# Kernel tuning notes

Hardware: AMD Instinct MI355X
Metric: run time of the kernel (lower is better)

## Reference

```python
import jax, jax.numpy as jnp
import numpy as np
import math

B, T, C, H, LC, DFF = 2, 1024, 1024, 16, 256, 4096
EPS = 1e-6


def _ln(x):
    # LayerNorm without affine (elementwise_affine=False under AdaLN), eps=1e-6
    m = jnp.mean(x, -1, keepdims=True)
    v = jnp.mean((x - m) ** 2, -1, keepdims=True)
    return (x - m) * jax.lax.rsqrt(v + EPS)


def _heads(t):
    b, l, c = t.shape
    return t.reshape(b, l, H, c // H).transpose(0, 2, 1, 3)  # (b,H,l,dh)


def _unheads(t):
    b, h, l, d = t.shape
    return t.transpose(0, 2, 1, 3).reshape(b, l, h * d)


def setup_inputs():
    key = jax.random.key(0)
    ks = jax.random.split(key, 16)
    s = 0.02
    p = lambda k, sh: jax.random.normal(k, sh, jnp.float32) * s
    x_star = jax.random.normal(ks[0], (B, T, C), jnp.float32)
    x_hat = jax.random.normal(ks[1], (B, T, C), jnp.float32)
    c = jax.random.normal(ks[2], (B, LC, C), jnp.float32)
    chunk = jnp.sort(jax.random.randint(ks[3], (B, T), 0, 32), axis=1)
    m_star = chunk[:, :, None] > chunk[:, None, :]   # attend to strictly earlier chunks
    m_hat = chunk[:, :, None] == chunk[:, None, :]   # attend within same chunk
    dep_mask = jax.random.bernoulli(ks[4], 0.98, (B, T, T)) | jnp.eye(T, dtype=bool)[None]
    return dict(
        x_star=x_star, x_hat=x_hat, c=c,
        m_star=m_star, m_hat=m_hat, dep_mask=dep_mask,
        ncond_g=jnp.ones((C,), jnp.float32), ncond_b=jnp.zeros((C,), jnp.float32),
        Wq=p(ks[5], (C, C)), bq=jnp.zeros((C,), jnp.float32),
        Wkv=p(ks[6], (C, 2 * C)), bkv=jnp.zeros((2 * C,), jnp.float32),
        Wco=p(ks[7], (C, C)), bco=jnp.zeros((C,), jnp.float32),
        Wada=p(ks[8], (C, 6 * C)), bada=jnp.zeros((6 * C,), jnp.float32),
        Wqkv=p(ks[9], (C, 3 * C)), bqkv=jnp.zeros((3 * C,), jnp.float32),
        Wo=p(ks[10], (C, C)), bo=jnp.zeros((C,), jnp.float32),
        W1=p(ks[11], (C, DFF)), b1=jnp.zeros((DFF,), jnp.float32),
        W2=p(ks[12], (DFF, C)), b2=jnp.zeros((C,), jnp.float32),
    )


def _cross_attn(x, c, Wq, bq, Wkv, bkv, Wco, bco):
    q = _heads(x @ Wq + bq)
    k, v = jnp.split(c @ Wkv + bkv, 2, -1)
    k, v = _heads(k), _heads(v)
    att = jnp.einsum('bhtd,bhsd->bhts', q, k) / math.sqrt(C // H)
    y = jnp.einsum('bhts,bhsd->bhtd', jax.nn.softmax(att, -1), v)
    return _unheads(y) @ Wco + bco


def _interleave(xs, xh, m_star, m_hat, dep, Wqkv, bqkv, Wo, bo):
    # Attention.forward_interleave (eval: dropout identity)
    NEG = -jnp.inf
    sc = 1.0 / math.sqrt(C // H)
    qkv = lambda x: [_heads(t) for t in jnp.split(x @ Wqkv + bqkv, 3, -1)]
    qs, ks, vs = qkv(xs)
    qh, kh, vh = qkv(xh)
    blk_star = (~m_star)[:, None]     # True -> block
    blk_hat = (~m_hat)[:, None]
    blk_dep = (~dep)[:, None]
    causal = jnp.triu(jnp.ones((T, T), bool), 1)[None, None]
    # star stream: causal + dependency mask
    att_star = jnp.einsum('bhtd,bhsd->bhts', qs, ks) * sc
    att_star = jnp.where(blk_dep, NEG, att_star)
    p_star = jax.nn.softmax(jnp.where(causal, NEG, att_star), -1)
    y_star = _unheads(jnp.einsum('bhts,bhsd->bhtd', p_star, vs)) @ Wo + bo
    # hat stream: merge logits (q_hat vs k_star on earlier chunks, q_hat vs k_hat within chunk)
    a1 = jnp.where(blk_star, NEG, jnp.einsum('bhtd,bhsd->bhts', qh, ks) * sc)
    a2 = jnp.where(blk_hat, NEG, jnp.einsum('bhtd,bhsd->bhts', qh, kh) * sc)
    merged = jnp.where(jnp.isinf(a2), a1, a2)
    merged = jnp.where(blk_dep, NEG, merged)
    p_hat = jax.nn.softmax(merged, -1)
    y_hat = jnp.einsum('bhts,bhsd->bhtd', jnp.where(blk_star, 0.0, p_hat), vs) \
          + jnp.einsum('bhts,bhsd->bhtd', jnp.where(blk_hat, 0.0, p_hat), vh)
    y_hat = _unheads(y_hat) @ Wo + bo
    return y_star, y_hat


def reference(x_star, x_hat, c, m_star, m_hat, dep_mask,
              ncond_g, ncond_b, Wq, bq, Wkv, bkv, Wco, bco, Wada, bada,
              Wqkv, bqkv, Wo, bo, W1, b1, W2, b2):
    mod = lambda x, sh, scale: x * (1 + scale) + sh
    mlp = lambda x: jax.nn.gelu(x @ W1 + b1, approximate=True) @ W2 + b2
    ca = lambda x: _cross_attn(_ln(x) * ncond_g + ncond_b, c, Wq, bq, Wkv, bkv, Wco, bco)
    ada = lambda t: jnp.split(jax.nn.silu(t) @ Wada + bada, 6, -1)
    gs = ada(ca(x_star))
    gh = ada(ca(x_hat))
    ms = mod(_ln(x_star), gs[0], gs[1])
    mh = mod(_ln(x_hat), gh[0], gh[1])
    ys, yh = _interleave(ms, mh, m_star, m_hat, dep_mask, Wqkv, bqkv, Wo, bo)
    x_star = x_star + gs[2] * ys
    x_hat = x_hat + gh[2] * yh
    x_star = x_star + gs[5] * mlp(mod(_ln(x_star), gs[3], gs[4]))
    x_hat = x_hat + gh[5] * mlp(mod(_ln(x_hat), gh[3], gh[4]))
    return x_star, x_hat
```

## Files before the change

### kernel.cpp

```cpp
#include <hip/hip_runtime.h>
#include <hip/hip_bf16.h>
#include <stdint.h>

#define DEVI __device__ __forceinline__

typedef __bf16 bf16x8 __attribute__((ext_vector_type(8)));
typedef float f32x4 __attribute__((ext_vector_type(4)));
typedef unsigned short us;
typedef unsigned long long ull;

DEVI float b2f(us u) { union { unsigned int i; float f; } v; v.i = ((unsigned int)u) << 16; return v.f; }
DEVI us f2b(float f) {
  union { unsigned int i; float f; } v; v.f = f;
  unsigned int r = (v.i + 0x7fffu + ((v.i >> 16) & 1u)) >> 16;
  return (us)r;
}

#define NEGINF (-__builtin_inff())

DEVI void gl2lds16(const us* g, us* l) {
  __builtin_amdgcn_global_load_lds(
      (const __attribute__((address_space(1))) unsigned int*)g,
      (__attribute__((address_space(3))) unsigned int*)l, 16, 0, 0);
}

__global__ __launch_bounds__(256) void detect_flags(
    const unsigned int* __restrict__ xw, const unsigned int* __restrict__ mw,
    int* __restrict__ flags) {
  const int t = threadIdx.x;
  int cnt = 0, big = 0;
  for (int i = t; i < 4096; i += 256) {
    unsigned int w = xw[i];
    us lo = (us)(w & 0xffffu);
    float a = fabsf(b2f(lo));
    cnt += ((lo == 0) || (a >= 1e-8f && a <= 256.f)) ? 1 : 0;
    big |= (mw[i] > 1u) ? 1 : 0;
  }
  for (int o = 32; o; o >>= 1) { cnt += __shfl_down(cnt, o); big |= __shfl_down(big, o); }
  __shared__ int sc[4], sb[4];
  if ((t & 63) == 0) { sc[t >> 6] = cnt; sb[t >> 6] = big; }
  __syncthreads();
  if (t == 0) {
    flags[0] = (sc[0] + sc[1] + sc[2] + sc[3] < 2048) ? 1 : 0;
    flags[1] = (sb[0] | sb[1] | sb[2] | sb[3]);
  }
}

__global__ __launch_bounds__(256) void cvt_bf16(
    const void* __restrict__ src, us* __restrict__ dst, int n,
    const int* __restrict__ flags) {
  const int f32mode = flags[0];
  int idx = (blockIdx.x * 256 + threadIdx.x) * 4;
  if (idx >= n) return;
  if (f32mode) {
    const float* s = (const float*)src;
    float4 v = *(const float4*)(s + idx);
    dst[idx] = f2b(v.x); dst[idx + 1] = f2b(v.y);
    dst[idx + 2] = f2b(v.z); dst[idx + 3] = f2b(v.w);
  } else {
    *(uint2*)(dst + idx) = *(const uint2*)((const us*)src + idx);
  }
}

struct P10 { const void* p[10]; };
__global__ __launch_bounds__(256) void cvt_small(P10 ps, us* __restrict__ dst,
                                                 const int* __restrict__ flags) {
  const int offs[11] = {0, 1024, 2048, 3072, 5120, 6144, 12288, 15360, 16384, 20480, 21504};
  int idx = blockIdx.x * 256 + threadIdx.x;
  if (idx >= 21504) return;
  int seg = 0;
#pragma unroll
  for (int i = 1; i < 10; ++i) seg += (idx >= offs[i]) ? 1 : 0;
  int local = idx - offs[seg];
  float v = flags[0] ? ((const float*)ps.p[seg])[local]
                     : b2f(((const us*)ps.p[seg])[local]);
  dst[idx] = f2b(v);
}

__global__ __launch_bounds__(256) void transpose_cvt64(
    const void* __restrict__ W, us* __restrict__ WT, int K, int N,
    const int* __restrict__ flags) {
  __shared__ __attribute__((aligned(16))) us tile[64 * 72];
  const int f32m = flags[0];
  const int k0 = blockIdx.x * 64, n0 = blockIdx.y * 64;
  const int t = threadIdx.x;
  const int row = t >> 2, colb = (t & 3) * 16;
  const int sw = ((row >> 4) & 3) << 4;
  us tmp[16];
  if (f32m) {
    const float* src = (const float*)W + (size_t)(k0 + row) * N + n0 + colb;
#pragma unroll
    for (int i = 0; i < 16; i += 4) {
      float4 v = *(const float4*)(src + i);
      tmp[i] = f2b(v.x); tmp[i + 1] = f2b(v.y); tmp[i + 2] = f2b(v.z); tmp[i + 3] = f2b(v.w);
    }
  } else {
    const us* src = (const us*)W + (size_t)(k0 + row) * N + n0 + colb;
    *(uint4*)tmp = *(const uint4*)src;
    *(uint4*)(tmp + 8) = *(const uint4*)(src + 8);
  }
  *(uint4*)&tile[row * 72 + (colb ^ sw)] = *(uint4*)tmp;
  *(uint4*)&tile[row * 72 + (colb ^ sw) + 8] = *(uint4*)(tmp + 8);
  __syncthreads();
  const int orow = t >> 2, ocolb = (t & 3) * 16;
  const int pc = (orow & 15) | ((orow & 48) ^ (ocolb & 48));
  us out[16];
#pragma unroll
  for (int i = 0; i < 16; ++i) out[i] = tile[(ocolb + i) * 72 + pc];
  us* dst = WT + (size_t)(n0 + orow) * K + k0 + ocolb;
  *(uint4*)dst = *(uint4*)out;
  *(uint4*)(dst + 8) = *(uint4*)(out + 8);
}

struct P3 { const void* p[3]; };
__global__ __launch_bounds__(256) void pack_mask3(P3 ms, ull* __restrict__ bits,
                                                  const int* __restrict__ flags) {
  const int bytemode = flags[1];
  const void* m = ms.p[blockIdx.y];
  ull* out = bits + (size_t)blockIdx.y * 32768;
  int wv = blockIdx.x * 4 + (threadIdx.x >> 6);
  int lane = threadIdx.x & 63;
  for (int w = 0; w < 16; ++w) {
    int v;
    if (bytemode) v = ((const unsigned char*)m)[(size_t)wv * 1024 + w * 64 + lane];
    else          v = ((const int*)m)[(size_t)wv * 1024 + w * 64 + lane];
    ull b = __ballot(v != 0);
    if (lane == 0) out[(size_t)wv * 16 + w] = b;
  }
}

__global__ __launch_bounds__(256) void hat_blockflags(
    const ull* __restrict__ starb, const ull* __restrict__ hatb, int* __restrict__ bf) {
  const int bt = blockIdx.x;
  const int b = bt >> 4, tt = bt & 15;
  const int t = threadIdx.x, wv = t >> 6, lane = t & 63;
  const int t0 = tt * 64;
  for (int k = 0; k < 4; ++k) {
    int ck = wv * 4 + k;
    ull sw = starb[(size_t)(b * 1024 + t0 + lane) * 16 + ck];
    ull hw = hatb[(size_t)(b * 1024 + t0 + lane) * 16 + ck];
    int f = (__ballot(sw != 0ull) ? 1 : 0) | (__ballot(hw != 0ull) ? 2 : 0);
    if (lane == 0) bf[bt * 16 + ck] = f;
  }
}

__global__ __launch_bounds__(256) void vtrans(
    const us* __restrict__ src, us* __restrict__ dst,
    int T, int stride, int colBase, int rowOff) {
  __shared__ __attribute__((aligned(16))) us tile[64][65];
  const int bh = blockIdx.y, b = bh >> 4, h = bh & 15;
  const int t0 = blockIdx.x * 64;
  const int t = threadIdx.x;
#pragma unroll
  for (int it = 0; it < 2; ++it) {
    int idx = it * 256 + t; int r = idx >> 3, c8 = (idx & 7) * 8;
    uint4 d4 = *(const uint4*)(src + (size_t)(rowOff + b * T + t0 + r) * stride + colBase + h * 64 + c8);
    const us* e = (const us*)&d4;
#pragma unroll
    for (int i = 0; i < 8; ++i) tile[r][c8 + i] = e[i];
  }
  __syncthreads();
#pragma unroll
  for (int it = 0; it < 2; ++it) {
    int idx = it * 256 + t; int d = idx >> 3, c8 = (idx & 7) * 8;
    us tmp[8];
#pragma unroll
    for (int i = 0; i < 8; ++i) tmp[i] = tile[c8 + i][d];
    *(uint4*)(dst + ((size_t)(bh * 64 + d)) * T + t0 + c8) = *(const uint4*)tmp;
  }
}

__global__ __launch_bounds__(256) void vtrans_qkv(
    const us* __restrict__ src, us* __restrict__ dst0, us* __restrict__ dst1) {
  __shared__ __attribute__((aligned(16))) us tile[64][65];
  const int z = blockIdx.z;
  us* dst = z ? dst1 : dst0;
  const int rowOff = z ? 2048 : 0;
  const int bh = blockIdx.y, b = bh >> 4, h = bh & 15;
  const int t0 = blockIdx.x * 64;
  const int t = threadIdx.x;
#pragma unroll
  for (int it = 0; it < 2; ++it) {
    int idx = it * 256 + t; int r = idx >> 3, c8 = (idx & 7) * 8;
    uint4 d4 = *(const uint4*)(src + (size_t)(rowOff + b * 1024 + t0 + r) * 3072 + 2048 + h * 64 + c8);
    const us* e = (const us*)&d4;
#pragma unroll
    for (int i = 0; i < 8; ++i) tile[r][c8 + i] = e[i];
  }
  __syncthreads();
#pragma unroll
  for (int it = 0; it < 2; ++it) {
    int idx = it * 256 + t; int d = idx >> 3, c8 = (idx & 7) * 8;
    us tmp[8];
#pragma unroll
    for (int i = 0; i < 8; ++i) tmp[i] = tile[c8 + i][d];
    *(uint4*)(dst + ((size_t)(bh * 64 + d)) * 1024 + t0 + c8) = *(const uint4*)tmp;
  }
}

__global__ __launch_bounds__(256) void ln_affine(
    const void* __restrict__ xs, const void* __restrict__ xh,
    const us* __restrict__ gw, const us* __restrict__ bw,
    us* __restrict__ lnx, us* __restrict__ xn, const int* __restrict__ flags) {
  const int f32m = flags[0];
  const int row = blockIdx.x;
  const void* xp = (row < 2048) ? xs : xh;
  const size_t base = (size_t)(row & 2047) * 1024;
  const int t = threadIdx.x;
  float v[4]; float s = 0.f, ss = 0.f;
#pragma unroll
  for (int i = 0; i < 4; ++i) {
    size_t idx = base + i * 256 + t;
    float x = f32m ? ((const float*)xp)[idx] : b2f(((const us*)xp)[idx]);
    v[i] = x; s += x; ss += x * x;
  }
  for (int o = 32; o; o >>= 1) { s += __shfl_down(s, o); ss += __shfl_down(ss, o); }
  __shared__ float red[2][4];
  const int wv = t >> 6, lane = t & 63;
  if (lane == 0) { red[0][wv] = s; red[1][wv] = ss; }
  __syncthreads();
  s = red[0][0] + red[0][1] + red[0][2] + red[0][3];
  ss = red[1][0] + red[1][1] + red[1][2] + red[1][3];
  const float mean = s * (1.f / 1024.f);
  const float var = fmaxf(ss * (1.f / 1024.f) - mean * mean, 0.f);
  const float rstd = rsqrtf(var + 1e-6f);
  const size_t ro = (size_t)row * 1024;
#pragma unroll
  for (int i = 0; i < 4; ++i) {
    int c = i * 256 + t;
    float n = (v[i] - mean) * rstd;
    lnx[ro + c] = f2b(n);
    xn[ro + c] = f2b(n * b2f(gw[c]) + b2f(bw[c]));
  }
}

__global__ __launch_bounds__(256) void mod_ms(
    const us* __restrict__ lnx, const us* __restrict__ gada, us* __restrict__ ms) {
  const size_t idx = ((size_t)blockIdx.x * 256 + threadIdx.x) * 4;
  const int row = (int)(idx >> 10), c = (int)(idx & 1023);
  const size_t gb = (size_t)row * 6144;
#pragma unroll
  for (int i = 0; i < 4; ++i) {
    float sh = b2f(gada[gb + c + i]);
    float sc = b2f(gada[gb + 1024 + c + i]);
    ms[idx + i] = f2b(b2f(lnx[idx + i]) * (1.f + sc) + sh);
  }
}

__global__ __launch_bounds__(256) void ln_mod(
    const float* __restrict__ x1, const us* __restrict__ gada, us* __restrict__ m2) {
  const int row = blockIdx.x;
  const float* xp = x1 + (size_t)row * 1024;
  const int t = threadIdx.x;
  float v[4]; float s = 0.f, ss = 0.f;
#pragma unroll
  for (int i = 0; i < 4; ++i) { float x = xp[i * 256 + t]; v[i] = x; s += x; ss += x * x; }
  for (int o = 32; o; o >>= 1) { s += __shfl_down(s, o); ss += __shfl_down(ss, o); }
  __shared__ float red[2][4];
  const int wv = t >> 6, lane = t & 63;
  if (lane == 0) { red[0][wv] = s; red[1][wv] = ss; }
  __syncthreads();
  s = red[0][0] + red[0][1] + red[0][2] + red[0][3];
  ss = red[1][0] + red[1][1] + red[1][2] + red[1][3];
  const float mean = s * (1.f / 1024.f);
  const float var = fmaxf(ss * (1.f / 1024.f) - mean * mean, 0.f);
  const float rstd = rsqrtf(var + 1e-6f);
  const size_t gb = (size_t)row * 6144;
#pragma unroll
  for (int i = 0; i < 4; ++i) {
    int c = i * 256 + t;
    float n = (v[i] - mean) * rstd;
    float sh = b2f(gada[gb + 3072 + c]);
    float sc = b2f(gada[gb + 4096 + c]);
    m2[(size_t)row * 1024 + c] = f2b(n * (1.f + sc) + sh);
  }
}

enum { EPI_BF16 = 0, EPI_SILU, EPI_GELU, EPI_GATE_XRES, EPI_GATE_OUT };

template <int EPI>
DEVI void gemm_epi(float v, int gmr, int gn, int N, void* out,
                   const us* gate, const void* res0, const void* res1,
                   const int* oflags) {
  const size_t oi = (size_t)gmr * N + gn;
  if constexpr (EPI == EPI_BF16) {
    ((us*)out)[oi] = f2b(v);
  } else if constexpr (EPI == EPI_SILU) {
    ((us*)out)[oi] = f2b(v / (1.f + __expf(-v)));
  } else if constexpr (EPI == EPI_GELU) {
    float u = 0.7978845608028654f * (v + 0.044715f * v * v * v);
    float th = 1.f - 2.f / (__expf(2.f * u) + 1.f);
    ((us*)out)[oi] = f2b(0.5f * v * (1.f + th));
  } else if constexpr (EPI == EPI_GATE_XRES) {
    float g = b2f(gate[(size_t)gmr * 6144 + gn]);
    const void* xr = (gmr < 2048) ? res0 : res1;
    size_t xi = (size_t)(gmr & 2047) * 1024 + gn;
    float x = oflags[0] ? ((const float*)xr)[xi] : b2f(((const us*)xr)[xi]);
    ((float*)out)[oi] = x + g * v;
  } else {
    float g = b2f(gate[(size_t)gmr * 6144 + gn]);
    float x = ((const float*)res0)[oi];
    float r2 = x + g * v;
    if (oflags[0]) ((float*)out)[oi] = r2;
    else ((us*)out)[oi] = f2b(r2);
  }
}

template <int EPI>
__global__ __launch_bounds__(256) void gemm_bt(
    const us* __restrict__ A, const us* __restrict__ BT,
    const us* __restrict__ bias, void* __restrict__ out,
    int M, int N, int K,
    const us* __restrict__ gate,
    const void* __restrict__ res0, const void* __restrict__ res1,
    const int* __restrict__ oflags) {
  __shared__ __attribute__((aligned(16))) us As[2][128 * 32];
  __shared__ __attribute__((aligned(16))) us Bs[2][128 * 32];
  const int m0 = blockIdx.x * 128, n0 = blockIdx.y * 128;
  const int t = threadIdx.x;
  const int wave = t >> 6, lane = t & 63;
  const int wm = (wave >> 1) * 64, wn = (wave & 1) * 64;
  const int l16 = lane & 15, quad = lane >> 4;
  f32x4 acc[4][4] = {};

  const int lr = lane >> 2, lc = (lane & 3) * 8;
  const us* gA = A + (size_t)(m0 + wave * 32 + lr) * K + lc;
  const us* gB = BT + (size_t)(n0 + wave * 32 + lr) * K + lc;
  const int wo = wave * 1024;

#define STAGE_BT(buf, k)                                    \
  { us* pA = &As[buf][wo]; us* pB = &Bs[buf][wo];           \
    gl2lds16(gA + (k), pA);                                 \
    gl2lds16(gA + (size_t)16 * K + (k), pA + 512);          \
    gl2lds16(gB + (k), pB);                                 \
    gl2lds16(gB + (size_t)16 * K + (k), pB + 512); }

  STAGE_BT(0, 0);
  STAGE_BT(1, 32);
  const int NK = K >> 5;
  int cur = 0;
  for (int i = 0; i < NK - 1; ++i) {
    asm volatile("s_waitcnt vmcnt(4)\n\ts_barrier" ::: "memory");
    bf16x8 af[4], bfv[4];
#pragma unroll
    for (int x = 0; x < 4; ++x) af[x] = *(const bf16x8*)(const void*)&As[cur][(wm + x * 16 + l16) * 32 + quad * 8];
#pragma unroll
    for (int j = 0; j < 4; ++j) bfv[j] = *(const bf16x8*)(const void*)&Bs[cur][(wn + j * 16 + l16) * 32 + quad * 8];
    asm volatile("s_waitcnt lgkmcnt(0)\n\ts_barrier" ::: "memory");
    if (i + 2 < NK) STAGE_BT(cur, (i + 2) * 32);
#pragma unroll
    for (int x = 0; x < 4; ++x)
#pragma unroll
      for (int j = 0; j < 4; ++j)
        acc[x][j] = __builtin_amdgcn_mfma_f32_16x16x32_bf16(af[x], bfv[j], acc[x][j], 0, 0, 0);
    cur ^= 1;
  }
  asm volatile("s_waitcnt vmcnt(0)\n\ts_barrier" ::: "memory");
  {
    bf16x8 af[4], bfv[4];
#pragma unroll
    for (int x = 0; x < 4; ++x) af[x] = *(const bf16x8*)(const void*)&As[cur][(wm + x * 16 + l16) * 32 + quad * 8];
#pragma unroll
    for (int j = 0; j < 4; ++j) bfv[j] = *(const bf16x8*)(const void*)&Bs[cur][(wn + j * 16 + l16) * 32 + quad * 8];
#pragma unroll
    for (int x = 0; x < 4; ++x)
#pragma unroll
      for (int j = 0; j < 4; ++j)
        acc[x][j] = __builtin_amdgcn_mfma_f32_16x16x32_bf16(af[x], bfv[j], acc[x][j], 0, 0, 0);
  }
#undef STAGE_BT

#pragma unroll
  for (int i = 0; i < 4; ++i) {
    const int gm = m0 + wm + i * 16 + quad * 4;
#pragma unroll
    for (int j = 0; j < 4; ++j) {
      const int gn = n0 + wn + j * 16 + l16;
      const float bv = b2f(bias[gn]);
#pragma unroll
      for (int r = 0; r < 4; ++r)
        gemm_epi<EPI>(acc[i][j][r] + bv, gm + r, gn, N, out, gate, res0, res1, oflags);
    }
  }
}

template <int EPI>
__global__ __launch_bounds__(256) void gemm_bt64(
    const us* __restrict__ A, const us* __restrict__ BT,
    const us* __restrict__ bias, void* __restrict__ out,
    int M, int N, int K,
    const us* __restrict__ gate,
    const void* __restrict__ res0, const void* __restrict__ res1,
    const int* __restrict__ oflags) {
  __shared__ __attribute__((aligned(16))) us As[2][128 * 32];
  __shared__ __attribute__((aligned(16))) us Bs[2][64 * 32];
  const int m0 = blockIdx.x * 128, n0 = blockIdx.y * 64;
  const int t = threadIdx.x;
  const int wave = t >> 6, lane = t & 63;
  const int wm = (wave >> 1) * 64, wn = (wave & 1) * 32;
  const int l16 = lane & 15, quad = lane >> 4;
  f32x4 acc[4][2] = {};

  const int lr = lane >> 2, lc = (lane & 3) * 8;
  const us* gA = A + (size_t)(m0 + wave * 32 + lr) * K + lc;
  const us* gB = BT + (size_t)(n0 + wave * 16 + lr) * K + lc;
  const int woA = wave * 1024, woB = wave * 512;

#define STAGE_BT64(buf, k)                                  \
  { us* pA = &As[buf][woA];                                 \
    gl2lds16(gA + (k), pA);                                 \
    gl2lds16(gA + (size_t)16 * K + (k), pA + 512);          \
    gl2lds16(gB + (k), &Bs[buf][woB]); }

  STAGE_BT64(0, 0);
  STAGE_BT64(1, 32);
  const int NK = K >> 5;
  int cur = 0;
  for (int i = 0; i < NK - 1; ++i) {
    asm volatile("s_waitcnt vmcnt(3)\n\ts_barrier" ::: "memory");
    bf16x8 af[4], bfv[2];
#pragma unroll
    for (int x = 0; x < 4; ++x) af[x] = *(const bf16x8*)(const void*)&As[cur][(wm + x * 16 + l16) * 32 + quad * 8];
#pragma unroll
    for (int j = 0; j < 2; ++j) bfv[j] = *(const bf16x8*)(const void*)&Bs[cur][(wn + j * 16 + l16) * 32 + quad * 8];
    asm volatile("s_waitcnt lgkmcnt(0)\n\ts_barrier" ::: "memory");
    if (i + 2 < NK) STAGE_BT64(cur, (i + 2) * 32);
#pragma unroll
    for (int x = 0; x < 4; ++x)
#pragma unroll
      for (int j = 0; j < 2; ++j)
        acc[x][j] = __builtin_amdgcn_mfma_f32_16x16x32_bf16(af[x], bfv[j], acc[x][j], 0, 0, 0);
    cur ^= 1;
  }
  asm volatile("s_waitcnt vmcnt(0)\n\ts_barrier" ::: "memory");
  {
    bf16x8 af[4], bfv[2];
#pragma unroll
    for (int x = 0; x < 4; ++x) af[x] = *(const bf16x8*)(const void*)&As[cur][(wm + x * 16 + l16) * 32 + quad * 8];
#pragma unroll
    for (int j = 0; j < 2; ++j) bfv[j] = *(const bf16x8*)(const void*)&Bs[cur][(wn + j * 16 + l16) * 32 + quad * 8];
#pragma unroll
    for (int x = 0; x < 4; ++x)
#pragma unroll
      for (int j = 0; j < 2; ++j)
        acc[x][j] = __builtin_amdgcn_mfma_f32_16x16x32_bf16(af[x], bfv[j], acc[x][j], 0, 0, 0);
  }
#undef STAGE_BT64

#pragma unroll
  for (int i = 0; i < 4; ++i) {
    const int gm = m0 + wm + i * 16 + quad * 4;
#pragma unroll
    for (int j = 0; j < 2; ++j) {
      const int gn = n0 + wn + j * 16 + l16;
      const float bv = b2f(bias[gn]);
#pragma unroll
      for (int r = 0; r < 4; ++r)
        gemm_epi<EPI>(acc[i][j][r] + bv, gm + r, gn, N, out, gate, res0, res1, oflags);
    }
  }
}

struct AttnState { float m[4], l[4]; f32x4 o[4]; };

DEVI void st_init(AttnState& s) {
#pragma unroll
  for (int r = 0; r < 4; ++r) { s.m[r] = NEGINF; s.l[r] = 0.f; s.o[r] = f32x4{}; }
}

DEVI void stage64(us* __restrict__ dst, const us* __restrict__ src,
                  int strideUs, int t) {
#pragma unroll
  for (int it = 0; it < 2; ++it) {
    const int id = it * 256 + t;
    const int row = id >> 3, c8 = (id & 7) * 8;
    *(uint4*)&dst[row * 72 + c8] = *(const uint4*)(src + (size_t)row * strideUs + c8);
  }
}

template <bool MASKED>
DEVI void attn_round(const us* __restrict__ Kb, const us* __restrict__ Vb,
                     us* __restrict__ Pb, const ull* mrow,
                     bf16x8 aq0, bf16x8 aq1, AttnState& st,
                     int wv, int l16, int quad) {
  f32x4 s[4];
  __builtin_amdgcn_s_setprio(1);
#pragma unroll
  for (int j = 0; j < 4; ++j) {
    const int row = j * 16 + l16;
    bf16x8 bk0 = *(const bf16x8*)(const void*)&Kb[row * 72 + quad * 8];
    bf16x8 bk1 = *(const bf16x8*)(const void*)&Kb[row * 72 + 32 + quad * 8];
    f32x4 z = {};
    z = __builtin_amdgcn_mfma_f32_16x16x32_bf16(aq0, bk0, z, 0, 0, 0);
    z = __builtin_amdgcn_mfma_f32_16x16x32_bf16(aq1, bk1, z, 0, 0, 0);
    s[j] = z;
  }
  __builtin_amdgcn_s_setprio(0);
  const float CE = 0.18033688011112042f;
#pragma unroll
  for (int r = 0; r < 4; ++r) {
    float mx = fmaxf(fmaxf(s[0][r], s[1][r]), fmaxf(s[2][r], s[3][r]));
#pragma unroll
    for (int o2 = 8; o2; o2 >>= 1) mx = fmaxf(mx, __shfl_xor(mx, o2));
    const float mn = fmaxf(st.m[r], mx);
    const float alpha = exp2f((st.m[r] - mn) * CE);
    const float mnC = mn * CE;
    float rs = 0.f;
#pragma unroll
    for (int j = 0; j < 4; ++j) {
      float p = exp2f(__builtin_fmaf(s[j][r], CE, -mnC));
      if constexpr (MASKED) p = ((mrow[r] >> (j * 16 + l16)) & 1ull) ? p : 0.f;
      rs += p;
      ((__bf16*)Pb)[(wv * 16 + quad * 4 + r) * 72 + j * 16 + l16] = (__bf16)p;
    }
#pragma unroll
    for (int o2 = 8; o2; o2 >>= 1) rs += __shfl_xor(rs, o2);
    st.m[r] = mn;
    st.l[r] = st.l[r] * alpha + rs;
#pragma unroll
    for (int jd = 0; jd < 4; ++jd) st.o[jd][r] *= alpha;
  }
  bf16x8 ap0 = *(const bf16x8*)(const void*)&Pb[(wv * 16 + l16) * 72 + quad * 8];
  bf16x8 ap1 = *(const bf16x8*)(const void*)&Pb[(wv * 16 + l16) * 72 + 32 + quad * 8];
  __builtin_amdgcn_s_setprio(1);
#pragma unroll
  for (int jd = 0; jd < 4; ++jd) {
    bf16x8 v0 = *(const bf16x8*)(const void*)&Vb[(jd * 16 + l16) * 72 + quad * 8];
    bf16x8 v1 = *(const bf16x8*)(const void*)&Vb[(jd * 16 + l16) * 72 + 32 + quad * 8];
    st.o[jd] = __builtin_amdgcn_mfma_f32_16x16x32_bf16(ap0, v0, st.o[jd], 0, 0, 0);
    st.o[jd] = __builtin_amdgcn_mfma_f32_16x16x32_bf16(ap1, v1, st.o[jd], 0, 0, 0);
  }
  __builtin_amdgcn_s_setprio(0);
}

DEVI void attn_write(us* __restrict__ y, const AttnState& st, int rowAbs,
                     int h, int l16, int quad) {
#pragma unroll
  for (int r = 0; r < 4; ++r) {
    const float inv = (st.l[r] > 0.f) ? 1.f / st.l[r] : 0.f;
#pragma unroll
    for (int jd = 0; jd < 4; ++jd)
      y[(size_t)(rowAbs + quad * 4 + r) * 1024 + h * 64 + jd * 16 + l16] =
          f2b(st.o[jd][r] * inv);
  }
}

__global__ __launch_bounds__(256) void cross_attn_mfma(
    const us* __restrict__ q, const us* __restrict__ kv,
    const us* __restrict__ vT, us* __restrict__ y) {
  __shared__ __attribute__((aligned(16))) us Kb[64 * 72];
  __shared__ __attribute__((aligned(16))) us Vb[64 * 72];
  __shared__ __attribute__((aligned(16))) us Pb[64 * 72];
  const int bid = blockIdx.x;
  const int xcd = bid & 7, tmp = bid >> 3;
  const int tt = tmp & 15, gq = tmp >> 4;
  const int g = gq * 8 + xcd;
  const int strm = g >> 5, b = (g >> 4) & 1, h = g & 15;
  const int t = threadIdx.x, wv = t >> 6, lane = t & 63;
  const int l16 = lane & 15, quad = lane >> 4;
  const int rowbase = strm * 2048 + b * 1024 + tt * 64 + wv * 16;
  const us* qp = q + (size_t)(rowbase + l16) * 1024 + h * 64 + quad * 8;
  bf16x8 aq0 = *(const bf16x8*)(qp);
  bf16x8 aq1 = *(const bf16x8*)(qp + 32);
  const us* kb = kv + (size_t)b * (256 * 2048) + h * 64;
  const us* vb = vT + (size_t)(b * 16 + h) * (64 * 256);
  AttnState st; st_init(st);
  for (int rnd = 0; rnd < 4; ++rnd) {
    const int s0 = rnd * 64;
    __syncthreads();
    stage64(Kb, kb + (size_t)s0 * 2048, 2048, t);
    stage64(Vb, vb + s0, 256, t);
    __syncthreads();
    attn_round<false>(Kb, Vb, Pb, nullptr, aq0, aq1, st, wv, l16, quad);
  }
  attn_write(y, st, rowbase, h, l16, quad);
}

DEVI void star_body(us* Kb, us* Vb, us* Pb, const us* qkv, const us* vT,
                    const ull* depb, us* y, int b, int h, int tt, int t) {
  const int wv = t >> 6, lane = t & 63;
  const int l16 = lane & 15, quad = lane >> 4;
  const int t0 = tt * 64;
  const int rowbase = b * 1024 + t0 + wv * 16;
  const us* qp = qkv + (size_t)(rowbase + l16) * 3072 + h * 64 + quad * 8;
  bf16x8 aq0 = *(const bf16x8*)(qp);
  bf16x8 aq1 = *(const bf16x8*)(qp + 32);
  const us* kb = qkv + (size_t)(b * 1024) * 3072 + 1024 + h * 64;
  const us* vb = vT + (size_t)(b * 16 + h) * 65536;
  AttnState st; st_init(st);
  ull mrow[4];
  for (int ck = 0; ck <= tt; ++ck) {
    const int s0 = ck * 64;
    __syncthreads();
    stage64(Kb, kb + (size_t)s0 * 3072, 3072, t);
    stage64(Vb, vb + s0, 1024, t);
    __syncthreads();
#pragma unroll
    for (int r = 0; r < 4; ++r) {
      ull d = depb[(size_t)(rowbase + quad * 4 + r) * 16 + ck];
      if (ck == tt) {
        const int idx = wv * 16 + quad * 4 + r;
        d &= (2ull << idx) - 1ull;
      }
      mrow[r] = d;
    }
    attn_round<true>(Kb, Vb, Pb, mrow, aq0, aq1, st, wv, l16, quad);
  }
  attn_write(y, st, rowbase, h, l16, quad);
}

DEVI void hat_body(us* Kb, us* Vb, us* Pb, const us* qkv,
                   const us* vsT, const us* vhT,
                   const ull* starb, const ull* hatb, const ull* depb,
                   const int* bflags, us* y, int b, int h, int tt, int t) {
  const int wv = t >> 6, lane = t & 63;
  const int l16 = lane & 15, quad = lane >> 4;
  const int t0 = tt * 64;
  const int rowbase = b * 1024 + t0 + wv * 16;
  const us* qp = qkv + (size_t)(2048 + rowbase + l16) * 3072 + h * 64 + quad * 8;
  bf16x8 aq0 = *(const bf16x8*)(qp);
  bf16x8 aq1 = *(const bf16x8*)(qp + 32);
  const us* ksb = qkv + (size_t)(b * 1024) * 3072 + 1024 + h * 64;
  const us* khb = qkv + (size_t)(2048 + b * 1024) * 3072 + 1024 + h * 64;
  const us* vsb = vsT + (size_t)(b * 16 + h) * 65536;
  const us* vhb = vhT + (size_t)(b * 16 + h) * 65536;
  AttnState st; st_init(st);
  ull mrow[4];
  for (int ck = 0; ck < 16; ++ck) {
    const int f = bflags[(b * 16 + tt) * 16 + ck];
    const int s0 = ck * 64;
    if (f & 1) {
      __syncthreads();
      stage64(Kb, ksb + (size_t)s0 * 3072, 3072, t);
      stage64(Vb, vsb + s0, 1024, t);
      __syncthreads();
#pragma unroll
      for (int r = 0; r < 4; ++r) {
        const size_t mi = (size_t)(rowbase + quad * 4 + r) * 16 + ck;
        mrow[r] = starb[mi] & depb[mi];
      }
      attn_round<true>(Kb, Vb, Pb, mrow, aq0, aq1, st, wv, l16, quad);
    }
    if (f & 2) {
      __syncthreads();
      stage64(Kb, khb + (size_t)s0 * 3072, 3072, t);
      stage64(Vb, vhb + s0, 1024, t);
      __syncthreads();
#pragma unroll
      for (int r = 0; r < 4; ++r) {
        const size_t mi = (size_t)(rowbase + quad * 4 + r) * 16 + ck;
        mrow[r] = hatb[mi] & depb[mi];
      }
      attn_round<true>(Kb, Vb, Pb, mrow, aq0, aq1, st, wv, l16, quad);
    }
  }
  attn_write(y, st, 2048 + rowbase, h, l16, quad);
}

__global__ __launch_bounds__(256) void self_attn_mfma(
    const us* __restrict__ qkv,
    const us* __restrict__ vstT, const us* __restrict__ vhtT,
    const ull* __restrict__ sbits, const ull* __restrict__ hbits,
    const ull* __restrict__ dbits, const int* __restrict__ bflags,
    us* __restrict__ y) {
  __shared__ __attribute__((aligned(16))) us Kb[64 * 72];
  __shared__ __attribute__((aligned(16))) us Vb[64 * 72];
  __shared__ __attribute__((aligned(16))) us Pb[64 * 72];
  const int bid = blockIdx.x;
  const int xcd = bid & 7, tmp = bid >> 3;
  const int pr = tmp & 7, gq = tmp >> 3;
  const int g = gq * 8 + xcd;
  const int ttA = pr, ttB = 15 - pr;
  const int t = threadIdx.x;
  if (g < 32) {
    star_body(Kb, Vb, Pb, qkv, vstT, dbits, y, g >> 4, g & 15, ttA, t);
    star_body(Kb, Vb, Pb, qkv, vstT, dbits, y, g >> 4, g & 15, ttB, t);
  } else {
    const int g2 = g - 32;
    hat_body(Kb, Vb, Pb, qkv, vstT, vhtT, sbits, hbits, dbits, bflags,
             y, g2 >> 4, g2 & 15, ttA, t);
    hat_body(Kb, Vb, Pb, qkv, vstT, vhtT, sbits, hbits, dbits, bflags,
             y, g2 >> 4, g2 & 15, ttB, t);
  }
}

extern "C" void kernel_launch(void* const* d_in, const int* in_sizes, int n_in,
                              void* d_out, int out_size, void* d_ws, size_t ws_size,
                              hipStream_t stream) {
  const void* xs = d_in[0];
  const void* xh = d_in[1];
  const void* cc = d_in[2];
  const void* mstar = d_in[3];
  const void* mhat = d_in[4];
  const void* mdep = d_in[5];
  const void* ng = d_in[6];
  const void* nb = d_in[7];
  const void* Wq = d_in[8];
  const void* bq = d_in[9];
  const void* Wkv = d_in[10];
  const void* bkv = d_in[11];
  const void* Wco = d_in[12];
  const void* bco = d_in[13];
  const void* Wada = d_in[14];
  const void* bada = d_in[15];
  const void* Wqkv = d_in[16];
  const void* bqkv = d_in[17];
  const void* Wo = d_in[18];
  const void* bo = d_in[19];
  const void* W1 = d_in[20];
  const void* b1 = d_in[21];
  const void* W2 = d_in[22];
  const void* b2 = d_in[23];
  (void)in_sizes; (void)n_in; (void)out_size; (void)ws_size;

  char* ws = (char*)d_ws;
  size_t off = 0;
  auto alloc = [&](size_t bytes) -> char* {
    char* p = ws + off;
    off += (bytes + 255) & ~(size_t)255;
    return p;
  };
  int* flags = (int*)alloc(256);
  int* bflags = (int*)alloc(512 * 4);
  us* smallb = (us*)alloc(21504 * 2);
  us* ngb = smallb, *nbb = smallb + 1024, *bqb = smallb + 2048,
      *bkvb = smallb + 3072, *bcob = smallb + 5120, *badab = smallb + 6144,
      *bqkvb = smallb + 12288, *bob = smallb + 15360, *b1b = smallb + 16384,
      *b2b = smallb + 20480;
  us* WqT = (us*)alloc(1048576ull * 2);
  us* WkvT = (us*)alloc(2097152ull * 2);
  us* WcoT = (us*)alloc(1048576ull * 2);
  us* WadaT = (us*)alloc(6291456ull * 2);
  us* WqkvT = (us*)alloc(3145728ull * 2);
  us* WoT = (us*)alloc(1048576ull * 2);
  us* W1T = (us*)alloc(4194304ull * 2);
  us* W2T = (us*)alloc(4194304ull * 2);
  us* xn = (us*)alloc(4194304ull * 2);
  us* qb = (us*)alloc(4194304ull * 2);
  us* kvb = (us*)alloc(1048576ull * 2);
  us* gada = (us*)alloc(25165824ull * 2);
  us* msb = (us*)alloc(4194304ull * 2);
  us* qkvb = (us*)alloc(12582912ull * 2);
  float* x1 = (float*)alloc(4194304ull * 4);
  us* hid = (us*)alloc(16777216ull * 2);
  ull* mb = (ull*)alloc(3ull * 32768 * 8);
  us* kvT = (us*)alloc(524288ull * 2);
  us* vstT = (us*)alloc(2097152ull * 2);
  us* vhtT = (us*)alloc(2097152ull * 2);

  ull* sbits = mb;
  ull* hbits = mb + 32768;
  ull* dbits = mb + 65536;
  us* ccb = hid;
  us* lnx = hid + 1048576;
  us* yca = xn;
  us* silub = qb;
  us* yat = msb;

  dim3 blk(256);
  detect_flags<<<1, blk, 0, stream>>>((const unsigned int*)xs, (const unsigned int*)mdep, flags);

  cvt_bf16<<<512, blk, 0, stream>>>(cc, ccb, 524288, flags);
  P10 ps10; ps10.p[0] = ng; ps10.p[1] = nb; ps10.p[2] = bq; ps10.p[3] = bkv;
  ps10.p[4] = bco; ps10.p[5] = bada; ps10.p[6] = bqkv; ps10.p[7] = bo;
  ps10.p[8] = b1; ps10.p[9] = b2;
  cvt_small<<<84, blk, 0, stream>>>(ps10, smallb, flags);

  transpose_cvt64<<<dim3(16, 16), blk, 0, stream>>>(Wq, WqT, 1024, 1024, flags);
  transpose_cvt64<<<dim3(16, 32), blk, 0, stream>>>(Wkv, WkvT, 1024, 2048, flags);
  transpose_cvt64<<<dim3(16, 16), blk, 0, stream>>>(Wco, WcoT, 1024, 1024, flags);
  transpose_cvt64<<<dim3(16, 96), blk, 0, stream>>>(Wada, WadaT, 1024, 6144, flags);
  transpose_cvt64<<<dim3(16, 48), blk, 0, stream>>>(Wqkv, WqkvT, 1024, 3072, flags);
  transpose_cvt64<<<dim3(16, 16), blk, 0, stream>>>(Wo, WoT, 1024, 1024, flags);
  transpose_cvt64<<<dim3(16, 64), blk, 0, stream>>>(W1, W1T, 1024, 4096, flags);
  transpose_cvt64<<<dim3(64, 16), blk, 0, stream>>>(W2, W2T, 4096, 1024, flags);

  P3 ps3; ps3.p[0] = mstar; ps3.p[1] = mhat; ps3.p[2] = mdep;
  pack_mask3<<<dim3(512, 3), blk, 0, stream>>>(ps3, mb, flags);
  hat_blockflags<<<32, blk, 0, stream>>>(sbits, hbits, bflags);

  ln_affine<<<4096, blk, 0, stream>>>(xs, xh, ngb, nbb, lnx, xn, flags);
  gemm_bt64<EPI_BF16><<<dim3(32, 16), blk, 0, stream>>>(xn, WqT, bqb, qb, 4096, 1024, 1024, nullptr, nullptr, nullptr, nullptr);
  gemm_bt64<EPI_BF16><<<dim3(4, 32), blk, 0, stream>>>(ccb, WkvT, bkvb, kvb, 512, 2048, 1024, nullptr, nullptr, nullptr, nullptr);
  vtrans<<<dim3(4, 32), blk, 0, stream>>>(kvb, kvT, 256, 2048, 1024, 0);
  cross_attn_mfma<<<1024, blk, 0, stream>>>(qb, kvb, kvT, yca);
  gemm_bt64<EPI_SILU><<<dim3(32, 16), blk, 0, stream>>>(yca, WcoT, bcob, silub, 4096, 1024, 1024, nullptr, nullptr, nullptr, nullptr);
  gemm_bt<EPI_BF16><<<dim3(32, 48), blk, 0, stream>>>(silub, WadaT, badab, gada, 4096, 6144, 1024, nullptr, nullptr, nullptr, nullptr);
  mod_ms<<<4096, blk, 0, stream>>>(lnx, gada, msb);
  gemm_bt<EPI_BF16><<<dim3(32, 24), blk, 0, stream>>>(msb, WqkvT, bqkvb, qkvb, 4096, 3072, 1024, nullptr, nullptr, nullptr, nullptr);
  vtrans_qkv<<<dim3(16, 32, 2), blk, 0, stream>>>(qkvb, vstT, vhtT);
  self_attn_mfma<<<512, blk, 0, stream>>>(qkvb, vstT, vhtT, sbits, hbits, dbits, bflags, yat);
  gemm_bt64<EPI_GATE_XRES><<<dim3(32, 16), blk, 0, stream>>>(yat, WoT, bob, x1, 4096, 1024, 1024, gada + 2048, xs, xh, flags);
  ln_mod<<<4096, blk, 0, stream>>>(x1, gada, msb);
  gemm_bt<EPI_GELU><<<dim3(32, 32), blk, 0, stream>>>(msb, W1T, b1b, hid, 4096, 4096, 1024, nullptr, nullptr, nullptr, nullptr);
  gemm_bt<EPI_GATE_OUT><<<dim3(32, 8), blk, 0, stream>>>(hid, W2T, b2b, d_out, 4096, 1024, 4096, gada + 5120, x1, nullptr, flags);
}
```

Measured before the change: 639.9 us.

## Double-buffer attention K/V via direct global-to-LDS loads with XOR swizzle

Cross- and self-attention kernels now stage K/V tiles with global_load_lds into double-buffered, XOR-swizzled LDS, prefetching the next tile while the current one is computed. This replaces the two barriers and register round-trip of each round with a single waitcnt plus barrier. The hat path precomputes a bitmask of active chunks so prefetch can run across them. The final W2 GEMM also switches to the 64-tile GEMM variant with more blocks. LDS use rises from the double buffers, and the swizzle must match between the load and read sides.

Result: slower. 728.1 us (+13.8%).

```diff
diff --git a/kernel.cpp b/kernel.cpp
--- a/kernel.cpp
+++ b/kernel.cpp
@@ -468,13 +468,14 @@
   for (int r = 0; r < 4; ++r) { s.m[r] = NEGINF; s.l[r] = 0.f; s.o[r] = f32x4{}; }
 }
 
-DEVI void stage64(us* __restrict__ dst, const us* __restrict__ src,
-                  int strideUs, int t) {
-#pragma unroll
-  for (int it = 0; it < 2; ++it) {
-    const int id = it * 256 + t;
-    const int row = id >> 3, c8 = (id & 7) * 8;
-    *(uint4*)&dst[row * 72 + c8] = *(const uint4*)(src + (size_t)row * strideUs + c8);
+DEVI void stage_gl(us* __restrict__ lds, const us* __restrict__ gsrc,
+                   int strideUs, int wv, int lane) {
+  const int rb = lane >> 3, c8 = (lane & 7) * 8;
+  const int swz = rb * 8;
+#pragma unroll
+  for (int k = 0; k < 2; ++k) {
+    const int row = wv * 16 + k * 8 + rb;
+    gl2lds16(gsrc + (size_t)row * strideUs + (c8 ^ swz), lds + (wv * 2 + k) * 512);
   }
 }
 
@@ -488,8 +489,9 @@
 #pragma unroll
   for (int j = 0; j < 4; ++j) {
     const int row = j * 16 + l16;
-    bf16x8 bk0 = *(const bf16x8*)(const void*)&Kb[row * 72 + quad * 8];
-    bf16x8 bk1 = *(const bf16x8*)(const void*)&Kb[row * 72 + 32 + quad * 8];
+    const int sw = (row & 7) * 8;
+    bf16x8 bk0 = *(const bf16x8*)(const void*)&Kb[row * 64 + ((quad * 8) ^ sw)];
+    bf16x8 bk1 = *(const bf16x8*)(const void*)&Kb[row * 64 + ((32 + quad * 8) ^ sw)];
     f32x4 z = {};
     z = __builtin_amdgcn_mfma_f32_16x16x32_bf16(aq0, bk0, z, 0, 0, 0);
     z = __builtin_amdgcn_mfma_f32_16x16x32_bf16(aq1, bk1, z, 0, 0, 0);
@@ -525,8 +527,10 @@
   __builtin_amdgcn_s_setprio(1);
 #pragma unroll
   for (int jd = 0; jd < 4; ++jd) {
-    bf16x8 v0 = *(const bf16x8*)(const void*)&Vb[(jd * 16 + l16) * 72 + quad * 8];
-    bf16x8 v1 = *(const bf16x8*)(const void*)&Vb[(jd * 16 + l16) * 72 + 32 + quad * 8];
+    const int row = jd * 16 + l16;
+    const int sw = (row & 7) * 8;
+    bf16x8 v0 = *(const bf16x8*)(const void*)&Vb[row * 64 + ((quad * 8) ^ sw)];
+    bf16x8 v1 = *(const bf16x8*)(const void*)&Vb[row * 64 + ((32 + quad * 8) ^ sw)];
     st.o[jd] = __builtin_amdgcn_mfma_f32_16x16x32_bf16(ap0, v0, st.o[jd], 0, 0, 0);
     st.o[jd] = __builtin_amdgcn_mfma_f32_16x16x32_bf16(ap1, v1, st.o[jd], 0, 0, 0);
   }
@@ -548,8 +552,8 @@
 __global__ __launch_bounds__(256) void cross_attn_mfma(
     const us* __restrict__ q, const us* __restrict__ kv,
     const us* __restrict__ vT, us* __restrict__ y) {
-  __shared__ __attribute__((aligned(16))) us Kb[64 * 72];
-  __shared__ __attribute__((aligned(16))) us Vb[64 * 72];
+  __shared__ __attribute__((aligned(16))) us Kb[2][64 * 64];
+  __shared__ __attribute__((aligned(16))) us Vb[2][64 * 64];
   __shared__ __attribute__((aligned(16))) us Pb[64 * 72];
   const int bid = blockIdx.x;
   const int xcd = bid & 7, tmp = bid >> 3;
@@ -565,18 +569,24 @@
   const us* kb = kv + (size_t)b * (256 * 2048) + h * 64;
   const us* vb = vT + (size_t)(b * 16 + h) * (64 * 256);
   AttnState st; st_init(st);
+  __syncthreads();
+  stage_gl(Kb[0], kb, 2048, wv, lane);
+  stage_gl(Vb[0], vb, 256, wv, lane);
+  int cur = 0;
   for (int rnd = 0; rnd < 4; ++rnd) {
-    const int s0 = rnd * 64;
-    __syncthreads();
-    stage64(Kb, kb + (size_t)s0 * 2048, 2048, t);
-    stage64(Vb, vb + s0, 256, t);
-    __syncthreads();
-    attn_round<false>(Kb, Vb, Pb, nullptr, aq0, aq1, st, wv, l16, quad);
+    asm volatile("s_waitcnt vmcnt(0)\n\ts_barrier" ::: "memory");
+    if (rnd < 3) {
+      stage_gl(Kb[cur ^ 1], kb + (size_t)(rnd + 1) * 64 * 2048, 2048, wv, lane);
+      stage_gl(Vb[cur ^ 1], vb + (rnd + 1) * 64, 256, wv, lane);
+    }
+    attn_round<false>(Kb[cur], Vb[cur], Pb, nullptr, aq0, aq1, st, wv, l16, quad);
+    cur ^= 1;
   }
   attn_write(y, st, rowbase, h, l16, quad);
 }
 
-DEVI void star_body(us* Kb, us* Vb, us* Pb, const us* qkv, const us* vT,
+DEVI void star_body(us (*Kb)[4096], us (*Vb)[4096], us* Pb,
+                    const us* qkv, const us* vT,
                     const ull* depb, us* y, int b, int h, int tt, int t) {
   const int wv = t >> 6, lane = t & 63;
   const int l16 = lane & 15, quad = lane >> 4;
@@ -589,12 +599,16 @@
   const us* vb = vT + (size_t)(b * 16 + h) * 65536;
   AttnState st; st_init(st);
   ull mrow[4];
+  __syncthreads();
+  stage_gl(Kb[0], kb, 3072, wv, lane);
+  stage_gl(Vb[0], vb, 1024, wv, lane);
+  int cur = 0;
   for (int ck = 0; ck <= tt; ++ck) {
-    const int s0 = ck * 64;
-    __syncthreads();
-    stage64(Kb, kb + (size_t)s0 * 3072, 3072, t);
-    stage64(Vb, vb + s0, 1024, t);
-    __syncthreads();
+    asm volatile("s_waitcnt vmcnt(0)\n\ts_barrier" ::: "memory");
+    if (ck < tt) {
+      stage_gl(Kb[cur ^ 1], kb + (size_t)(ck + 1) * 64 * 3072, 3072, wv, lane);
+      stage_gl(Vb[cur ^ 1], vb + (ck + 1) * 64, 1024, wv, lane);
+    }
 #pragma unroll
     for (int r = 0; r < 4; ++r) {
       ull d = depb[(size_t)(rowbase + quad * 4 + r) * 16 + ck];
@@ -604,13 +618,14 @@
       }
       mrow[r] = d;
     }
-    attn_round<true>(Kb, Vb, Pb, mrow, aq0, aq1, st, wv, l16, quad);
+    attn_round<true>(Kb[cur], Vb[cur], Pb, mrow, aq0, aq1, st, wv, l16, quad);
+    cur ^= 1;
   }
   attn_write(y, st, rowbase, h, l16, quad);
 }
 
-DEVI void hat_body(us* Kb, us* Vb, us* Pb, const us* qkv,
-                   const us* vsT, const us* vhT,
+DEVI void hat_body(us (*Kb)[4096], us (*Vb)[4096], us* Pb,
+                   const us* qkv, const us* vsT, const us* vhT,
                    const ull* starb, const ull* hatb, const ull* depb,
                    const int* bflags, us* y, int b, int h, int tt, int t) {
   const int wv = t >> 6, lane = t & 63;
@@ -625,33 +640,42 @@
   const us* vsb = vsT + (size_t)(b * 16 + h) * 65536;
   const us* vhb = vhT + (size_t)(b * 16 + h) * 65536;
   AttnState st; st_init(st);
-  ull mrow[4];
+  unsigned mask = 0;
   for (int ck = 0; ck < 16; ++ck) {
-    const int f = bflags[(b * 16 + tt) * 16 + ck];
-    const int s0 = ck * 64;
-    if (f & 1) {
-      __syncthreads();
-      stage64(Kb, ksb + (size_t)s0 * 3072, 3072, t);
-      stage64(Vb, vsb + s0, 1024, t);
-      __syncthreads();
+    int f = bflags[(b * 16 + tt) * 16 + ck];
+    mask |= (unsigned)(f & 3) << (2 * ck);
+  }
+  if (mask) {
+    int slot = (int)__builtin_ctz(mask);
+    unsigned rem = mask & (mask - 1);
+    __syncthreads();
+    {
+      const int ck = slot >> 1, part = slot & 1;
+      stage_gl(Kb[0], (part ? khb : ksb) + (size_t)ck * 64 * 3072, 3072, wv, lane);
+      stage_gl(Vb[0], (part ? vhb : vsb) + ck * 64, 1024, wv, lane);
+    }
+    int cur = 0;
+    for (;;) {
+      asm volatile("s_waitcnt vmcnt(0)\n\ts_barrier" ::: "memory");
+      const int ck = slot >> 1, part = slot & 1;
+      int nslot = -1;
+      if (rem) {
+        nslot = (int)__builtin_ctz(rem);
+        rem &= rem - 1;
+        const int nck = nslot >> 1, npart = nslot & 1;
+        stage_gl(Kb[cur ^ 1], (npart ? khb : ksb) + (size_t)nck * 64 * 3072, 3072, wv, lane);
+        stage_gl(Vb[cur ^ 1], (npart ? vhb : vsb) + nck * 64, 1024, wv, lane);
+      }
+      ull mrow[4];
 #pragma unroll
       for (int r = 0; r < 4; ++r) {
         const size_t mi = (size_t)(rowbase + quad * 4 + r) * 16 + ck;
-        mrow[r] = starb[mi] & depb[mi];
+        mrow[r] = (part ? hatb[mi] : starb[mi]) & depb[mi];
       }
-      attn_round<true>(Kb, Vb, Pb, mrow, aq0, aq1, st, wv, l16, quad);
-    }
-    if (f & 2) {
-      __syncthreads();
-      stage64(Kb, khb + (size_t)s0 * 3072, 3072, t);
-      stage64(Vb, vhb + s0, 1024, t);
-      __syncthreads();
-#pragma unroll
-      for (int r = 0; r < 4; ++r) {
-        const size_t mi = (size_t)(rowbase + quad * 4 + r) * 16 + ck;
-        mrow[r] = hatb[mi] & depb[mi];
-      }
-      attn_round<true>(Kb, Vb, Pb, mrow, aq0, aq1, st, wv, l16, quad);
+      attn_round<true>(Kb[cur], Vb[cur], Pb, mrow, aq0, aq1, st, wv, l16, quad);
+      if (nslot < 0) break;
+      slot = nslot;
+      cur ^= 1;
     }
   }
   attn_write(y, st, 2048 + rowbase, h, l16, quad);
@@ -663,8 +687,8 @@
     const ull* __restrict__ sbits, const ull* __restrict__ hbits,
     const ull* __restrict__ dbits, const int* __restrict__ bflags,
     us* __restrict__ y) {
-  __shared__ __attribute__((aligned(16))) us Kb[64 * 72];
-  __shared__ __attribute__((aligned(16))) us Vb[64 * 72];
+  __shared__ __attribute__((aligned(16))) us Kb[2][64 * 64];
+  __shared__ __attribute__((aligned(16))) us Vb[2][64 * 64];
   __shared__ __attribute__((aligned(16))) us Pb[64 * 72];
   const int bid = blockIdx.x;
   const int xcd = bid & 7, tmp = bid >> 3;
@@ -793,5 +817,5 @@
   gemm_bt64<EPI_GATE_XRES><<<dim3(32, 16), blk, 0, stream>>>(yat, WoT, bob, x1, 4096, 1024, 1024, gada + 2048, xs, xh, flags);
   ln_mod<<<4096, blk, 0, stream>>>(x1, gada, msb);
   gemm_bt<EPI_GELU><<<dim3(32, 32), blk, 0, stream>>>(msb, W1T, b1b, hid, 4096, 4096, 1024, nullptr, nullptr, nullptr, nullptr);
-  gemm_bt<EPI_GATE_OUT><<<dim3(32, 8), blk, 0, stream>>>(hid, W2T, b2b, d_out, 4096, 1024, 4096, gada + 5120, x1, nullptr, flags);
-}
+  gemm_bt64<EPI_GATE_OUT><<<dim3(32, 16), blk, 0, stream>>>(hid, W2T, b2b, d_out, 4096, 1024, 4096, gada + 5120, x1, nullptr, flags);
+}
```
